# Kernel tuning notes

Measured on AMD Instinct MI355X. Metric: run time of the kernel, lower is better.

## Reference

```python
import jax, jax.numpy as jnp
import numpy as np

EPS = 1e-5

def _ln(x, g=None, b=None):
    m = jnp.mean(x, axis=-1, keepdims=True)
    v = jnp.var(x, axis=-1, keepdims=True)
    y = (x - m) / jnp.sqrt(v + EPS)
    if g is not None:
        y = y * g + b
    return y

def setup_inputs() -> dict:
    key = jax.random.key(0)
    B, N, C = 2, 2048, 1024   # batch, tokens, query_dim
    H, D = 16, 64             # heads, dim_head -> inner = 1024
    inner = H * D
    ks = jax.random.split(key, 8)
    s = C ** -0.5
    inp = {
        'x':   jax.random.normal(ks[0], (B, N, C), jnp.float32),
        'w_q': jax.random.normal(ks[1], (C, inner), jnp.float32) * s,
        'b_q': jnp.zeros((inner,), jnp.float32),
        'w_k': jax.random.normal(ks[2], (C, inner), jnp.float32) * s,
        'b_k': jnp.zeros((inner,), jnp.float32),
        'w_v': jax.random.normal(ks[3], (C, inner), jnp.float32) * s,
        'b_v': jnp.zeros((inner,), jnp.float32),
        'g_q': jnp.ones((inner,), jnp.float32),
        'be_q': jnp.zeros((inner,), jnp.float32),
        'g_k': jnp.ones((inner,), jnp.float32),
        'be_k': jnp.zeros((inner,), jnp.float32),
        # to_out is zero-initialized in the torch code; use small random weights
        # so forward/backward are non-trivial for correctness testing.
        'w_o': jax.random.normal(ks[4], (inner, C), jnp.float32) * s,
        'b_o': jnp.zeros((C,), jnp.float32),
    }
    return inp

def reference(x, w_q, b_q, w_k, b_k, w_v, b_v, g_q, be_q, g_k, be_k, w_o, b_o):
    B, N, C = x.shape
    inner = w_q.shape[1]
    H = 16
    D = inner // H
    xn = _ln(x)                                  # pre-norm, no affine
    ctx = xn                                     # self-attention (context=None)
    silu = jax.nn.silu
    q = silu(xn) @ w_q + b_q                     # [B,N,inner]
    k = silu(ctx) @ w_k + b_k
    v = silu(ctx) @ w_v + b_v
    q = _ln(q, g_q, be_q)
    k = _ln(k, g_k, be_k)
    q = q * (inner ** -0.5)                      # NB: scale by inner_dim, pre-split
    q = q.reshape(B, N, H, D)
    k = k.reshape(B, N, H, D)
    v = v.reshape(B, N, H, D)
    w = jnp.einsum('bihd,bjhd->bhij', q, k)      # [B,H,N,N]
    w = jax.nn.softmax(w, axis=-1)
    o = jnp.einsum('bhij,bjhd->bihd', w, v).reshape(B, N, inner)
    return silu(o) @ w_o + b_o
```

## Files before the change

### kernel.cpp

```cpp
#include <hip/hip_runtime.h>
#include <hip/hip_bf16.h>
#include <math.h>

#define LN_EPS 1e-5f

typedef __attribute__((ext_vector_type(8))) short bf16x8;
typedef __attribute__((ext_vector_type(8))) short short8;
typedef __attribute__((ext_vector_type(4))) float f32x4;
typedef unsigned short ushort_t;

__device__ __forceinline__ float silu_f(float x) {
    return x / (1.0f + __expf(-x));
}

__device__ __forceinline__ ushort_t f2bf(float f) {
    __hip_bfloat16 h = __float2bfloat16(f);
    return *reinterpret_cast<ushort_t*>(&h);
}

__device__ __forceinline__ float bf2f(ushort_t u) {
    __hip_bfloat16 h = *reinterpret_cast<__hip_bfloat16*>(&u);
    return __bfloat162float(h);
}

__device__ __forceinline__ unsigned pk2(float a, float b) {
#if defined(__has_builtin)
#if __has_builtin(__builtin_amdgcn_cvt_pk_bf16_f32)
    return __builtin_bit_cast(unsigned, __builtin_amdgcn_cvt_pk_bf16_f32(a, b));
#else
    return (((unsigned)f2bf(b)) << 16) | (unsigned)f2bf(a);
#endif
#else
    return (((unsigned)f2bf(b)) << 16) | (unsigned)f2bf(a);
#endif
}

__device__ __forceinline__ void gld16(const void* g, void* lds) {
    __builtin_amdgcn_global_load_lds(
        (const __attribute__((address_space(1))) unsigned int*)g,
        (__attribute__((address_space(3))) unsigned int*)lds, 16, 0, 0);
}

__device__ __forceinline__ float2 block_reduce2(float2 p, float2* sbuf) {
    #pragma unroll
    for (int off = 32; off > 0; off >>= 1) {
        p.x += __shfl_down(p.x, off, 64);
        p.y += __shfl_down(p.y, off, 64);
    }
    int lane = threadIdx.x & 63;
    int wid  = threadIdx.x >> 6;
    if (lane == 0) sbuf[wid] = p;
    __syncthreads();
    if (threadIdx.x == 0) {
        float2 r = sbuf[0];
        for (int i = 1; i < 4; ++i) { r.x += sbuf[i].x; r.y += sbuf[i].y; }
        sbuf[0] = r;
    }
    __syncthreads();
    return sbuf[0];
}

__global__ __launch_bounds__(256) void ln_silu_kernel(
    const float* __restrict__ x, ushort_t* __restrict__ out)
{
    __shared__ float2 sbuf[4];
    const int C = 1024;
    int row = blockIdx.x;
    const float4* xr = (const float4*)(x + (size_t)row * C);
    float4 v = xr[threadIdx.x];
    float2 p;
    p.x = v.x + v.y + v.z + v.w;
    p.y = v.x*v.x + v.y*v.y + v.z*v.z + v.w*v.w;
    float2 s = block_reduce2(p, sbuf);
    float mean = s.x / (float)C;
    float var  = s.y / (float)C - mean * mean;
    float rstd = rsqrtf(var + LN_EPS);
    ushort4 y;
    y.x = f2bf(silu_f((v.x - mean) * rstd));
    y.y = f2bf(silu_f((v.y - mean) * rstd));
    y.z = f2bf(silu_f((v.z - mean) * rstd));
    y.w = f2bf(silu_f((v.w - mean) * rstd));
    ((ushort4*)(out + (size_t)row * C))[threadIdx.x] = y;
}

__global__ __launch_bounds__(256) void ln_affine_bf16(
    ushort_t* __restrict__ qk0, ushort_t* __restrict__ qk1,
    const float* __restrict__ g0, const float* __restrict__ be0,
    const float* __restrict__ g1, const float* __restrict__ be1,
    float scale0, float scale1)
{
    __shared__ float2 sbuf[4];
    const int C = 1024;
    int which = blockIdx.y;
    ushort_t* q = which ? qk1 : qk0;
    const float* g  = which ? g1  : g0;
    const float* be = which ? be1 : be0;
    float scale = which ? scale1 : scale0;
    int row = blockIdx.x;
    ushort4 u = ((ushort4*)(q + (size_t)row * C))[threadIdx.x];
    float v0 = bf2f(u.x), v1 = bf2f(u.y), v2 = bf2f(u.z), v3 = bf2f(u.w);
    float2 p;
    p.x = v0 + v1 + v2 + v3;
    p.y = v0*v0 + v1*v1 + v2*v2 + v3*v3;
    float2 s = block_reduce2(p, sbuf);
    float mean = s.x / (float)C;
    float var  = s.y / (float)C - mean * mean;
    float rstd = rsqrtf(var + LN_EPS);
    float4 gv = ((const float4*)g)[threadIdx.x];
    float4 bv = ((const float4*)be)[threadIdx.x];
    ushort4 y;
    y.x = f2bf(((v0 - mean) * rstd * gv.x + bv.x) * scale);
    y.y = f2bf(((v1 - mean) * rstd * gv.y + bv.y) * scale);
    y.z = f2bf(((v2 - mean) * rstd * gv.z + bv.z) * scale);
    y.w = f2bf(((v3 - mean) * rstd * gv.w + bv.w) * scale);
    ((ushort4*)(q + (size_t)row * C))[threadIdx.x] = y;
}

struct W4 { const float* p[4]; };

__global__ __launch_bounds__(256) void transpose_w(W4 w, ushort_t* __restrict__ outbase)
{
    __shared__ float Ls[64][65];
    int z = blockIdx.z;
    const float* in = w.p[z];
    ushort_t* out = outbase + (size_t)z * 1024 * 1024;
    int r0 = blockIdx.y * 64, c0 = blockIdx.x * 64;
    int t = threadIdx.x, r = t >> 2, j = (t & 3) * 16;
    #pragma unroll
    for (int i = 0; i < 4; ++i) {
        float4 v = *(const float4*)(in + (size_t)(r0 + r) * 1024 + c0 + j + i * 4);
        Ls[r][j + i*4 + 0] = v.x;
        Ls[r][j + i*4 + 1] = v.y;
        Ls[r][j + i*4 + 2] = v.z;
        Ls[r][j + i*4 + 3] = v.w;
    }
    __syncthreads();
    __align__(16) ushort_t tmp[16];
    #pragma unroll
    for (int i = 0; i < 16; ++i) tmp[i] = f2bf(Ls[j + i][r]);
    ushort_t* op = out + (size_t)(c0 + r) * 1024 + r0 + j;
    *(short8*)(op)     = *(short8*)(tmp);
    *(short8*)(op + 8) = *(short8*)(tmp + 8);
}

template<int BM, bool OUT_BF16>
__global__ __launch_bounds__(256) void gemm_mfma(
    const ushort_t* __restrict__ A, const ushort_t* __restrict__ Bt0,
    const float* __restrict__ b0, const float* __restrict__ b1,
    const float* __restrict__ b2, void* __restrict__ out0,
    ushort_t* __restrict__ vt_out,
    int M, int N, int K)
{
    constexpr int BK = 64;
    constexpr int MI = BM / 32;
    __shared__ ushort_t Smem[(BM + 128) * BK];
    ushort_t* As = Smem;
    ushort_t* Bs = Smem + BM * BK;

    int z = blockIdx.z;
    const ushort_t* Bt = Bt0 + (size_t)z * N * K;
    const float* bias = (z == 0) ? b0 : (z == 1) ? b1 : b2;

    int t = threadIdx.x;
    int lane = t & 63, wv = t >> 6;
    int wr = wv >> 1, wc = wv & 1;
    int quad = lane >> 4, ln16 = lane & 15;

    int row0 = blockIdx.y * BM;
    int col0 = blockIdx.x * 128;

    const f32x4 zero4 = {0.f, 0.f, 0.f, 0.f};
    f32x4 acc[MI][4];
    #pragma unroll
    for (int i = 0; i < MI; ++i)
        #pragma unroll
        for (int j = 0; j < 4; ++j) acc[i][j] = zero4;

    for (int kt = 0; kt < K; kt += BK) {
        #pragma unroll
        for (int c = 0; c < BM / 32; ++c) {
            int idx = c * 256 + t;
            int r = idx >> 3, ch = idx & 7;
            int g = ch ^ (r & 7);
            gld16(A + (size_t)(row0 + r) * K + kt + g * 8,
                  As + (size_t)(c * 256 + wv * 64) * 8);
        }
        #pragma unroll
        for (int c = 0; c < 4; ++c) {
            int idx = c * 256 + t;
            int r = idx >> 3, ch = idx & 7;
            int g = ch ^ (r & 7);
            gld16(Bt + (size_t)(col0 + r) * K + kt + g * 8,
                  Bs + (size_t)(c * 256 + wv * 64) * 8);
        }
        __syncthreads();
        #pragma unroll
        for (int s = 0; s < 2; ++s) {
            bf16x8 af[MI], bf[4];
            int g = s * 4 + quad;
            #pragma unroll
            for (int i = 0; i < MI; ++i) {
                int m = wr * (BM / 2) + i * 16 + ln16;
                af[i] = *(const bf16x8*)(As + (size_t)(m * 8 + (g ^ (m & 7))) * 8);
            }
            #pragma unroll
            for (int j = 0; j < 4; ++j) {
                int n = wc * 64 + j * 16 + ln16;
                bf[j] = *(const bf16x8*)(Bs + (size_t)(n * 8 + (g ^ (n & 7))) * 8);
            }
            #pragma unroll
            for (int i = 0; i < MI; ++i)
                #pragma unroll
                for (int j = 0; j < 4; ++j)
                    acc[i][j] = __builtin_amdgcn_mfma_f32_16x16x32_bf16(
                        af[i], bf[j], acc[i][j], 0, 0, 0);
        }
        __syncthreads();
    }

    if (OUT_BF16 && z == 2 && BM == 128) {
        ushort_t* tb = Smem + wv * 4096;
        int tok0 = row0 + wr * 64;
        int chn0 = col0 + wc * 64;
        #pragma unroll
        for (int j = 0; j < 4; ++j) {
            int chl = j * 16 + ln16;
            float bv = bias[chn0 + chl];
            #pragma unroll
            for (int i = 0; i < MI; ++i) {
                uint2 uu;
                uu.x = pk2(acc[i][j][0] + bv, acc[i][j][1] + bv);
                uu.y = pk2(acc[i][j][2] + bv, acc[i][j][3] + bv);
                int hc = i * 4 + quad;
                int phys = hc ^ ((chl & 7) << 1);
                *(uint2*)(tb + chl * 64 + phys * 4) = uu;
            }
        }
        int bb2 = tok0 >> 11;
        int tokb = tok0 & 2047;
        #pragma unroll
        for (int p = 0; p < 8; ++p) {
            int chl = p * 8 + (lane >> 3);
            int tc  = lane & 7;
            int ptc = tc ^ (chl & 7);
            uint4 vvv = *(const uint4*)(tb + chl * 64 + ptc * 8);
            *(uint4*)(vt_out + ((size_t)bb2 * 1024 + chn0 + chl) * 2048 + tokb + tc * 8) = vvv;
        }
    } else {
        #pragma unroll
        for (int j = 0; j < 4; ++j) {
            int col = col0 + wc * 64 + j * 16 + ln16;
            float bv = bias[col];
            #pragma unroll
            for (int i = 0; i < MI; ++i) {
                int rowb = row0 + wr * (BM / 2) + i * 16 + quad * 4;
                #pragma unroll
                for (int r = 0; r < 4; ++r) {
                    float val = acc[i][j][r] + bv;
                    if (OUT_BF16) {
                        ushort_t* out = (ushort_t*)out0 + (size_t)z * M * N;
                        out[(size_t)(rowb + r) * N + col] = f2bf(val);
                    } else {
                        float* out = (float*)out0;
                        out[(size_t)(rowb + r) * N + col] = val;
                    }
                }
            }
        }
    }
}

__global__ __launch_bounds__(256, 4) void flash_mfma(
    const ushort_t* __restrict__ qb, const ushort_t* __restrict__ kb,
    const ushort_t* __restrict__ vT, ushort_t* __restrict__ ob)
{
    const int N = 2048, HD = 1024, D = 64, H = 16;
    const int KT = 128;
    __shared__ ushort_t Ks[128 * 64];
    __shared__ ushort_t Vs[64 * 128];

    int t = threadIdx.x, lane = t & 63, wv = t >> 6;
    int quad = lane >> 4, ln16 = lane & 15;
    int qt = blockIdx.x, h = blockIdx.y, b = blockIdx.z;

    size_t qk_base = (size_t)b * N * HD + (size_t)h * D;
    size_t vt_base = (size_t)(b * H + h) * D * N;

    bf16x8 qf[2];
    {
        const ushort_t* qp = qb + qk_base + (size_t)(qt * 64 + wv * 16 + ln16) * HD;
        qf[0] = *(const bf16x8*)(qp + quad * 8);
        qf[1] = *(const bf16x8*)(qp + 32 + quad * 8);
    }

    const f32x4 zero4 = {0.f, 0.f, 0.f, 0.f};
    f32x4 oacc[4];
    #pragma unroll
    for (int j = 0; j < 4; ++j) oacc[j] = zero4;
    float lcur = 0.f;

    for (int kt = 0; kt < N; kt += KT) {
        __syncthreads();
        #pragma unroll
        for (int c = 0; c < 4; ++c) {
            int idx = c * 256 + t;
            int r = idx >> 3, ch = idx & 7, g = ch ^ (r & 7);
            int pr = (r & ~31) | (((r >> 2) & 3) << 3) | (((r >> 4) & 1) << 2) | (r & 3);
            gld16(kb + qk_base + (size_t)(kt + pr) * HD + g * 8,
                  Ks + (size_t)(c * 256 + wv * 64) * 8);
        }
        #pragma unroll
        for (int c = 0; c < 4; ++c) {
            int idx = c * 256 + t;
            int r = idx >> 4, ch = idx & 15, g = ch ^ (r & 15);
            gld16(vT + vt_base + (size_t)r * N + kt + g * 8,
                  Vs + (size_t)(c * 256 + wv * 64) * 8);
        }
        __syncthreads();

        f32x4 st[8];
        #pragma unroll
        for (int j = 0; j < 8; ++j) st[j] = zero4;
        #pragma unroll
        for (int s = 0; s < 2; ++s) {
            int g = s * 4 + quad;
            #pragma unroll
            for (int j = 0; j < 8; ++j) {
                int n = j * 16 + ln16;
                bf16x8 kf = *(const bf16x8*)(Ks + ((size_t)n * 8 + (g ^ (n & 7))) * 8);
                st[j] = __builtin_amdgcn_mfma_f32_16x16x32_bf16(kf, qf[s], st[j], 0, 0, 0);
            }
        }

        #pragma unroll
        for (int j = 0; j < 8; ++j) {
            st[j][0] = exp2f(st[j][0]);
            st[j][1] = exp2f(st[j][1]);
            st[j][2] = exp2f(st[j][2]);
            st[j][3] = exp2f(st[j][3]);
            lcur += (st[j][0] + st[j][1]) + (st[j][2] + st[j][3]);
        }

        #pragma unroll
        for (int w = 0; w < 4; ++w) {
            uint4 up;
            up.x = pk2(st[2*w][0],   st[2*w][1]);
            up.y = pk2(st[2*w][2],   st[2*w][3]);
            up.z = pk2(st[2*w+1][0], st[2*w+1][1]);
            up.w = pk2(st[2*w+1][2], st[2*w+1][3]);
            bf16x8 pf = __builtin_bit_cast(bf16x8, up);
            int lc = w * 4 + quad;
            #pragma unroll
            for (int mt = 0; mt < 4; ++mt) {
                int dd = mt * 16 + ln16;
                int phys = lc ^ ln16;
                bf16x8 vf = *(const bf16x8*)(Vs + (size_t)dd * 128 + phys * 8);
                oacc[mt] = __builtin_amdgcn_mfma_f32_16x16x32_bf16(vf, pf, oacc[mt], 0, 0, 0);
            }
        }
    }

    lcur += __shfl_xor(lcur, 16, 64);
    lcur += __shfl_xor(lcur, 32, 64);

    float inv = 1.0f / lcur;
    size_t rowoff = qk_base + (size_t)(qt * 64 + wv * 16 + ln16) * HD;
    #pragma unroll
    for (int mt = 0; mt < 4; ++mt) {
        float o0 = silu_f(oacc[mt][0] * inv);
        float o1 = silu_f(oacc[mt][1] * inv);
        float o2 = silu_f(oacc[mt][2] * inv);
        float o3 = silu_f(oacc[mt][3] * inv);
        uint2 uu;
        uu.x = pk2(o0, o1);
        uu.y = pk2(o2, o3);
        *(uint2*)(ob + rowoff + mt * 16 + quad * 4) = uu;
    }
}

extern "C" void kernel_launch(void* const* d_in, const int* in_sizes, int n_in,
                              void* d_out, int out_size, void* d_ws, size_t ws_size,
                              hipStream_t stream) {
    const float* x    = (const float*)d_in[0];
    const float* w_q  = (const float*)d_in[1];
    const float* b_q  = (const float*)d_in[2];
    const float* w_k  = (const float*)d_in[3];
    const float* b_k  = (const float*)d_in[4];
    const float* w_v  = (const float*)d_in[5];
    const float* b_v  = (const float*)d_in[6];
    const float* g_q  = (const float*)d_in[7];
    const float* be_q = (const float*)d_in[8];
    const float* g_k  = (const float*)d_in[9];
    const float* be_k = (const float*)d_in[10];
    const float* w_o  = (const float*)d_in[11];
    const float* b_o  = (const float*)d_in[12];
    float* out = (float*)d_out;

    const int B = 2, N = 2048, C = 1024, H = 16, INNER = 1024;
    const int M = B * N;
    const size_t MC = (size_t)M * C;

    ushort_t* ws  = (ushort_t*)d_ws;
    ushort_t* sx  = ws;
    ushort_t* qkv = ws + MC;
    ushort_t* vTp = ws + 4 * MC;
    ushort_t* wT  = ws + 5 * MC;

    ushort_t* qbuf = qkv;
    ushort_t* kbuf = qkv + MC;
    ushort_t* obuf = sx;

    W4 w4; w4.p[0] = w_q; w4.p[1] = w_k; w4.p[2] = w_v; w4.p[3] = w_o;
    transpose_w<<<dim3(16, 16, 4), 256, 0, stream>>>(w4, wT);

    ln_silu_kernel<<<M, 256, 0, stream>>>(x, sx);

    gemm_mfma<128, true><<<dim3(INNER / 128, M / 128, 3), 256, 0, stream>>>(
        sx, wT, b_q, b_k, b_v, qkv, vTp, M, INNER, C);

    ln_affine_bf16<<<dim3(M, 2), 256, 0, stream>>>(
        qbuf, kbuf, g_q, be_q, g_k, be_k, 0.03125f * 1.44269504f, 1.0f);

    flash_mfma<<<dim3(N / 64, H, B), 256, 0, stream>>>(qbuf, kbuf, vTp, obuf);

    gemm_mfma<64, false><<<dim3(C / 128, M / 64, 1), 256, 0, stream>>>(
        obuf, wT + (size_t)3 * 1024 * 1024, b_o, b_o, b_o, out, nullptr, M, C, INNER);
}
```

Measured before the change: 240.9 us.

## Double-buffer K/V tiles in flash attention with async prefetch and MFMA priority

Shrinks the key tile from 128 to 64 rows and double-buffers K and V in shared memory, so the direct-to-LDS load of the next tile is issued before computing the current one and is waited on with vmcnt counters instead of full syncs. It also raises wave priority around the MFMA sections and adds scheduling barriers. The aim is to hide global load latency behind matrix work. In exchange there are more loop iterations with barriers and a fixed vmcnt count that depends on the exact number of loads per stage.

```diff
diff --git a/kernel.cpp b/kernel.cpp
--- a/kernel.cpp
+++ b/kernel.cpp
@@ -275,9 +275,10 @@
     const ushort_t* __restrict__ vT, ushort_t* __restrict__ ob)
 {
     const int N = 2048, HD = 1024, D = 64, H = 16;
-    const int KT = 128;
-    __shared__ ushort_t Ks[128 * 64];
-    __shared__ ushort_t Vs[64 * 128];
+    const int KT = 64;
+    const int NT = N / KT;
+    __shared__ ushort_t Ks[2][64 * 64];
+    __shared__ ushort_t Vs[2][64 * 64];
 
     int t = threadIdx.x, lane = t & 63, wv = t >> 6;
     int quad = lane >> 4, ln16 = lane & 15;
@@ -299,41 +300,43 @@
     for (int j = 0; j < 4; ++j) oacc[j] = zero4;
     float lcur = 0.f;
 
-    for (int kt = 0; kt < N; kt += KT) {
-        __syncthreads();
-        #pragma unroll
-        for (int c = 0; c < 4; ++c) {
+    auto stage_tile = [&](ushort_t* KsB, ushort_t* VsB, int kt) {
+        #pragma unroll
+        for (int c = 0; c < 2; ++c) {
             int idx = c * 256 + t;
             int r = idx >> 3, ch = idx & 7, g = ch ^ (r & 7);
             int pr = (r & ~31) | (((r >> 2) & 3) << 3) | (((r >> 4) & 1) << 2) | (r & 3);
             gld16(kb + qk_base + (size_t)(kt + pr) * HD + g * 8,
-                  Ks + (size_t)(c * 256 + wv * 64) * 8);
-        }
-        #pragma unroll
-        for (int c = 0; c < 4; ++c) {
+                  KsB + (size_t)(c * 256 + wv * 64) * 8);
+        }
+        #pragma unroll
+        for (int c = 0; c < 2; ++c) {
             int idx = c * 256 + t;
-            int r = idx >> 4, ch = idx & 15, g = ch ^ (r & 15);
+            int r = idx >> 3, ch = idx & 7, g = ch ^ (r & 7);
             gld16(vT + vt_base + (size_t)r * N + kt + g * 8,
-                  Vs + (size_t)(c * 256 + wv * 64) * 8);
-        }
-        __syncthreads();
-
-        f32x4 st[8];
-        #pragma unroll
-        for (int j = 0; j < 8; ++j) st[j] = zero4;
+                  VsB + (size_t)(c * 256 + wv * 64) * 8);
+        }
+    };
+
+    auto compute_tile = [&](const ushort_t* KsB, const ushort_t* VsB) {
+        f32x4 st[4];
+        #pragma unroll
+        for (int j = 0; j < 4; ++j) st[j] = zero4;
+        __builtin_amdgcn_s_setprio(1);
         #pragma unroll
         for (int s = 0; s < 2; ++s) {
             int g = s * 4 + quad;
             #pragma unroll
-            for (int j = 0; j < 8; ++j) {
+            for (int j = 0; j < 4; ++j) {
                 int n = j * 16 + ln16;
-                bf16x8 kf = *(const bf16x8*)(Ks + ((size_t)n * 8 + (g ^ (n & 7))) * 8);
+                bf16x8 kf = *(const bf16x8*)(KsB + ((size_t)n * 8 + (g ^ (n & 7))) * 8);
                 st[j] = __builtin_amdgcn_mfma_f32_16x16x32_bf16(kf, qf[s], st[j], 0, 0, 0);
             }
         }
-
-        #pragma unroll
-        for (int j = 0; j < 8; ++j) {
+        __builtin_amdgcn_s_setprio(0);
+
+        #pragma unroll
+        for (int j = 0; j < 4; ++j) {
             st[j][0] = exp2f(st[j][0]);
             st[j][1] = exp2f(st[j][1]);
             st[j][2] = exp2f(st[j][2]);
@@ -342,7 +345,7 @@
         }
 
         #pragma unroll
-        for (int w = 0; w < 4; ++w) {
+        for (int w = 0; w < 2; ++w) {
             uint4 up;
             up.x = pk2(st[2*w][0],   st[2*w][1]);
             up.y = pk2(st[2*w][2],   st[2*w][3]);
@@ -350,14 +353,39 @@
             up.w = pk2(st[2*w+1][2], st[2*w+1][3]);
             bf16x8 pf = __builtin_bit_cast(bf16x8, up);
             int lc = w * 4 + quad;
+            int phys = lc ^ (ln16 & 7);
+            __builtin_amdgcn_s_setprio(1);
             #pragma unroll
             for (int mt = 0; mt < 4; ++mt) {
                 int dd = mt * 16 + ln16;
-                int phys = lc ^ ln16;
-                bf16x8 vf = *(const bf16x8*)(Vs + (size_t)dd * 128 + phys * 8);
+                bf16x8 vf = *(const bf16x8*)(VsB + (size_t)dd * 64 + phys * 8);
                 oacc[mt] = __builtin_amdgcn_mfma_f32_16x16x32_bf16(vf, pf, oacc[mt], 0, 0, 0);
             }
-        }
+            __builtin_amdgcn_s_setprio(0);
+        }
+        __builtin_amdgcn_sched_barrier(0);
+    };
+
+    stage_tile(Ks[0], Vs[0], 0);
+    #pragma unroll 1
+    for (int it = 0; it < NT; it += 2) {
+        stage_tile(Ks[1], Vs[1], (it + 1) * KT);
+        asm volatile("s_waitcnt vmcnt(4)" ::: "memory");
+        __builtin_amdgcn_s_barrier();
+        __builtin_amdgcn_sched_barrier(0);
+        compute_tile(Ks[0], Vs[0]);
+        __builtin_amdgcn_s_barrier();
+
+        if (it + 2 < NT) {
+            stage_tile(Ks[0], Vs[0], (it + 2) * KT);
+            asm volatile("s_waitcnt vmcnt(4)" ::: "memory");
+        } else {
+            asm volatile("s_waitcnt vmcnt(0)" ::: "memory");
+        }
+        __builtin_amdgcn_s_barrier();
+        __builtin_amdgcn_sched_barrier(0);
+        compute_tile(Ks[1], Vs[1]);
+        __builtin_amdgcn_s_barrier();
     }
 
     lcur += __shfl_xor(lcur, 16, 64);
```

After: 240.8 us. About the same (-0.1%).
